# Kernel tuning notes

Hardware: AMD Instinct MI355X
Metric: run time of the kernel (lower is better)

Reference implementation:

```python
import jax, jax.numpy as jnp
import numpy as np

NP, NR, NK = 64, 8, 500          # problems, rollouts, candidate nodes
H, HEADS, VD = 256, 8, 8         # hidden_dim, heads, vars_dim
HD = H // HEADS                  # head_dim
CLIP = 10.0                      # tanh logit clipping
NEG_INF = -jnp.inf


def setup_inputs() -> dict:
    key = jax.random.key(0)
    ks = jax.random.split(key, 17)
    f = lambda k, s: jax.random.normal(k, s, dtype=jnp.float32)
    B = NP * NR
    s = 1.0 / np.sqrt(H)
    return {
        "X": f(ks[0], (NP, NK, H)),
        "K": f(ks[1], (HEADS, NP, NK, HD)),
        "V": f(ks[2], (HEADS, NP, NK, HD)),
        "query": f(ks[3], (B, H)),
        "state1": f(ks[4], (B, H)),
        "state2": f(ks[5], (B, H)),
        "varfeat": f(ks[6], (NP, VD, NK)),
        "mask": jax.random.uniform(ks[7], (NP, NR, NK)) < 0.1,
        "nn_Q": f(ks[8], (HEADS, H, HD)) * (1.0 / np.sqrt(HD)),
        "nn_O": f(ks[9], (H, H)) * s,
        "nn_A": f(ks[10], (VD, H)) * s,
        "nn_B": f(ks[11], (H,)) * s,
        "nn_W": f(ks[12], (H,)) * s,
        "W_ih": f(ks[13], (4 * H, H)) * s,
        "W_hh": f(ks[14], (4 * H, H)) * s,
        "b_ih": f(ks[15], (4 * H,)) * s,
        "b_hh": f(ks[16], (4 * H,)) * s,
    }


def _decode(X, K, V, query, state1, state2, varfeat, mask,
            nn_Q, nn_O, nn_A, nn_B, nn_W, W_ih, W_hh, b_ih, b_hh):
    B = query.shape[0]
    # --- LSTMCell (PyTorch gate order: i, f, g, o) ---
    gates = query @ W_ih.T + b_ih + state1 @ W_hh.T + b_hh
    i, fg, g, o = jnp.split(gates, 4, axis=1)
    c = jax.nn.sigmoid(fg) * state2 + jax.nn.sigmoid(i) * jnp.tanh(g)
    h = jax.nn.sigmoid(o) * jnp.tanh(c)
    # --- MultiHeadAttention (glimpse) ---
    q = h.reshape(NP, NR, H)
    Q = jnp.einsum('pqh,ahd->apqd', q, nn_Q)                    # [heads,NP,NR,HD]
    S = jnp.einsum('apqd,apkd->apqk', Q, K) * (1.0 / np.sqrt(HD))
    S = jnp.where(mask[None], NEG_INF, S)
    S = jax.nn.softmax(S, axis=-1)
    x = jnp.einsum('apqk,apkd->apqd', S, V)
    x = x.transpose(1, 2, 0, 3).reshape(NP, NR, H)              # [NP,NR,H]
    qm = x @ nn_O                                               # glimpse query
    # --- additive attention with variable features ---
    vf = jnp.einsum('pvk,vh->pkh', varfeat, nn_A) + nn_B        # [NP,NK,H]
    t = jnp.tanh(X[:, None] + vf[:, None] + qm[:, :, None])     # [NP,NR,NK,H]
    logit = jnp.einsum('pqkh,h->pqk', t, nn_W)
    logit = jnp.where(mask, NEG_INF, logit).reshape(B, NK)
    # --- choose (mode=1: greedy argmax) ---
    infeasible = logit == NEG_INF
    l = jnp.where(infeasible, NEG_INF, jnp.tanh(logit) * CLIP)
    chosen = jnp.argmax(l, axis=1)
    logp = jax.nn.log_softmax(l, axis=1)
    chosen_p = jnp.take_along_axis(logp, chosen[:, None], axis=1).squeeze(1)
    return h, c, chosen_p


def reference(X, K, V, query, state1, state2, varfeat, mask,
              nn_Q, nn_O, nn_A, nn_B, nn_W, W_ih, W_hh, b_ih, b_hh):
    return _decode(X, K, V, query, state1, state2, varfeat, mask,
                   nn_Q, nn_O, nn_A, nn_B, nn_W, W_ih, W_hh, b_ih, b_hh)
```

## Files before the change

kernel.cpp:

```cpp
#include <hip/hip_runtime.h>

#define NPP   64
#define NRR   8
#define NKK   500
#define HDIM  256
#define NHEAD 8
#define VDIM  8
#define HD    32
#define BTOT  512

__device__ __forceinline__ float fast_tanh(float x) {
  const float e = __expf(2.f * x);
  return 1.f - 2.f * __builtin_amdgcn_rcpf(e + 1.f);
}
__device__ __forceinline__ float fast_sig(float x) {
  return __builtin_amdgcn_rcpf(1.f + __expf(-x));
}

__global__ __launch_bounds__(128) void k_lstm5(
    const float* __restrict__ query, const float* __restrict__ state1,
    const float* __restrict__ state2,
    const float* __restrict__ W_ih, const float* __restrict__ W_hh,
    const float* __restrict__ b_ih, const float* __restrict__ b_hh,
    const unsigned char* __restrict__ maskb, int* __restrict__ flagp,
    float* __restrict__ out_h, float* __restrict__ out_c)
{
  __shared__ float Wt[32][36];
  __shared__ float At[32][68];
  __shared__ float gt[32][68];

  const int t  = threadIdx.x;
  const int hb = blockIdx.x;
  const int bb = blockIdx.y;

  if (flagp != nullptr && hb == 0 && bb == 0) {
    __shared__ int f;
    if (t == 0) f = 0;
    __syncthreads();
    int any = 0;
    for (int j = t; j < 2048; j += 128) any |= maskb[2 * j + 1];
    if (any) atomicOr(&f, 1);
    __syncthreads();
    if (t == 0) *flagp = f;
  }

  const int tr = t >> 4;
  const int tc = t & 15;

  const int grow = t >> 2;
  const int kseg = t & 3;
  const int wgrow = (grow >> 3) * HDIM + hb * 8 + (grow & 7);
  const int agrow0 = bb * 64 + grow;
  const int agrow1 = agrow0 + 32;

  float4 wr0, wr1, ar0, ar1, ar2, ar3;

#define LSTM_ISSUE(K0)                                                        \
  {                                                                           \
    const int k0_ = (K0);                                                     \
    const float* wsrc = (k0_ < 256)                                           \
        ? (W_ih + (size_t)wgrow * HDIM + k0_)                                 \
        : (W_hh + (size_t)wgrow * HDIM + (k0_ - 256));                        \
    wr0 = *reinterpret_cast<const float4*>(wsrc + kseg * 8);                  \
    wr1 = *reinterpret_cast<const float4*>(wsrc + kseg * 8 + 4);              \
    const float* asrc0 = (k0_ < 256)                                          \
        ? (query  + (size_t)agrow0 * HDIM + k0_)                              \
        : (state1 + (size_t)agrow0 * HDIM + (k0_ - 256));                     \
    ar0 = *reinterpret_cast<const float4*>(asrc0 + kseg * 8);                 \
    ar1 = *reinterpret_cast<const float4*>(asrc0 + kseg * 8 + 4);             \
    const float* asrc1 = (k0_ < 256)                                          \
        ? (query  + (size_t)agrow1 * HDIM + k0_)                              \
        : (state1 + (size_t)agrow1 * HDIM + (k0_ - 256));                     \
    ar2 = *reinterpret_cast<const float4*>(asrc1 + kseg * 8);                 \
    ar3 = *reinterpret_cast<const float4*>(asrc1 + kseg * 8 + 4);             \
  }

#define LSTM_WRITE()                                                          \
  {                                                                           \
    const float w0[4] = {wr0.x, wr0.y, wr0.z, wr0.w};                         \
    const float w1[4] = {wr1.x, wr1.y, wr1.z, wr1.w};                         \
    const float a0[4] = {ar0.x, ar0.y, ar0.z, ar0.w};                         \
    const float a1[4] = {ar1.x, ar1.y, ar1.z, ar1.w};                         \
    const float a2[4] = {ar2.x, ar2.y, ar2.z, ar2.w};                         \
    const float a3[4] = {ar3.x, ar3.y, ar3.z, ar3.w};                         \
    _Pragma("unroll")                                                         \
    for (int i = 0; i < 4; ++i) {                                             \
      Wt[kseg * 8 + i][grow]     = w0[i];                                     \
      Wt[kseg * 8 + 4 + i][grow] = w1[i];                                     \
      At[kseg * 8 + i][grow]     = a0[i];                                     \
      At[kseg * 8 + 4 + i][grow] = a1[i];                                     \
      At[kseg * 8 + i][grow + 32]     = a2[i];                                \
      At[kseg * 8 + 4 + i][grow + 32] = a3[i];                                \
    }                                                                         \
  }

  float acc[4][4];
#pragma unroll
  for (int i = 0; i < 4; ++i)
#pragma unroll
    for (int j = 0; j < 4; ++j) acc[i][j] = 0.f;

  LSTM_ISSUE(0);
  LSTM_WRITE();
  __syncthreads();

  for (int k0 = 0; k0 < 512; k0 += 32) {
    const bool more = (k0 + 32) < 512;
    if (more) LSTM_ISSUE(k0 + 32);

#pragma unroll 8
    for (int kk = 0; kk < 32; ++kk) {
      const float4 wv = *reinterpret_cast<const float4*>(&Wt[kk][tr * 4]);
      const float4 av = *reinterpret_cast<const float4*>(&At[kk][tc * 4]);
      const float w[4] = {wv.x, wv.y, wv.z, wv.w};
      const float a[4] = {av.x, av.y, av.z, av.w};
#pragma unroll
      for (int i = 0; i < 4; ++i)
#pragma unroll
        for (int j = 0; j < 4; ++j) acc[i][j] += w[i] * a[j];
    }
    __syncthreads();
    if (more) {
      LSTM_WRITE();
      __syncthreads();
    }
  }

#pragma unroll
  for (int i = 0; i < 4; ++i) {
    float4 v;
    v.x = acc[i][0]; v.y = acc[i][1]; v.z = acc[i][2]; v.w = acc[i][3];
    *reinterpret_cast<float4*>(&gt[tr * 4 + i][tc * 4]) = v;
  }
  __syncthreads();

#pragma unroll
  for (int it = 0; it < 4; ++it) {
    const int cell = t + 128 * it;
    const int h = cell & 7, b = cell >> 3;
    const int gh = hb * 8 + h;
    const int gb = bb * 64 + b;
    const float bi = b_ih[0 * HDIM + gh] + b_hh[0 * HDIM + gh];
    const float bf = b_ih[1 * HDIM + gh] + b_hh[1 * HDIM + gh];
    const float bg = b_ih[2 * HDIM + gh] + b_hh[2 * HDIM + gh];
    const float bo = b_ih[3 * HDIM + gh] + b_hh[3 * HDIM + gh];
    const float iv = fast_sig (gt[ 0 + h][b] + bi);
    const float fv = fast_sig (gt[ 8 + h][b] + bf);
    const float gv = fast_tanh(gt[16 + h][b] + bg);
    const float ov = fast_sig (gt[24 + h][b] + bo);
    const size_t off = (size_t)gb * HDIM + gh;
    const float c = fv * state2[off] + iv * gv;
    out_c[off] = c;
    out_h[off] = ov * fast_tanh(c);
  }
}

__global__ __launch_bounds__(512) void k_attn10(
    const float* __restrict__ Kt, const float* __restrict__ Vt,
    const float* __restrict__ nn_Q, const float* __restrict__ nn_O,
    const void* __restrict__ maskp, const int* __restrict__ flagp,
    const float* __restrict__ out_h, float* __restrict__ qm_slabs)
{
  const int p = blockIdx.x >> 3;
  const int a = blockIdx.x & 7;
  const int t = threadIdx.x;
  const int wave = t >> 6, lane = t & 63;

  __shared__ float hs[NRR][HDIM];
  __shared__ float Qs[NRR][36];
  __shared__ float Sb[NRR][512];
  __shared__ float pb[8][NRR][HD];
  __shared__ float xs[NRR][36];

  const float4 hv = reinterpret_cast<const float4*>(
      out_h + (size_t)p * NRR * HDIM)[t];

  const int flag = *flagp;

  const int kc = (t < NKK) ? t : (NKK - 1);
  const float4* kp4 = reinterpret_cast<const float4*>(
      Kt + (((size_t)a * NPP + p) * NKK + kc) * HD);
  float4 kreg[8];
#pragma unroll
  for (int j = 0; j < 8; ++j) kreg[j] = kp4[j];

  float maskv[NRR];
  {
    const unsigned char* mb = (const unsigned char*)maskp;
    const int* mi = (const int*)maskp;
#pragma unroll
    for (int r = 0; r < NRR; ++r) {
      const size_t mo = (size_t)(p * NRR + r) * NKK + kc;
      const bool mk = flag ? (mb[mo] != 0) : (mi[mo] != 0);
      maskv[r] = mk ? -INFINITY : 0.f;
    }
  }

  reinterpret_cast<float4*>(&hs[0][0])[t] = hv;
  __syncthreads();

  {
    const int r = wave;
    const int d4 = lane >> 3, ks = lane & 7;
    float qx = 0.f, qy = 0.f, qz = 0.f, qw = 0.f;
#pragma unroll
    for (int i = 0; i < 8; ++i) {
      const int hb = 32 * i + ks * 4;
      const float4 hv4 = *reinterpret_cast<const float4*>(&hs[r][hb]);
      const float hh[4] = {hv4.x, hv4.y, hv4.z, hv4.w};
      const float* nqb = nn_Q + ((size_t)a * HDIM + hb) * HD + d4 * 4;
#pragma unroll
      for (int jj = 0; jj < 4; ++jj) {
        const float4 wv = *reinterpret_cast<const float4*>(nqb + (size_t)jj * HD);
        qx += hh[jj] * wv.x; qy += hh[jj] * wv.y;
        qz += hh[jj] * wv.z; qw += hh[jj] * wv.w;
      }
    }
#pragma unroll
    for (int off = 1; off < 8; off <<= 1) {
      qx += __shfl_xor(qx, off, 64);
      qy += __shfl_xor(qy, off, 64);
      qz += __shfl_xor(qz, off, 64);
      qw += __shfl_xor(qw, off, 64);
    }
    if (ks == 0) {
      const float sc = 0.17677669529663687f;
      Qs[r][d4 * 4 + 0] = qx * sc; Qs[r][d4 * 4 + 1] = qy * sc;
      Qs[r][d4 * 4 + 2] = qz * sc; Qs[r][d4 * 4 + 3] = qw * sc;
    }
  }
  __syncthreads();

#pragma unroll
  for (int r = 0; r < NRR; ++r) {
    float s = 0.f;
#pragma unroll
    for (int j = 0; j < 8; ++j) {
      const float4 q = *reinterpret_cast<const float4*>(&Qs[r][j * 4]);
      const float4 k4 = kreg[j];
      s += q.x * k4.x + q.y * k4.y + q.z * k4.z + q.w * k4.w;
    }
    Sb[r][t] = (t < NKK) ? (s + maskv[r]) : -INFINITY;
  }

  const int kg = t >> 3;
  const int d4p = t & 7;
  float4 v4[8];
  {
    const float* vbase = Vt + ((size_t)a * NPP + p) * NKK * HD + d4p * 4;
#pragma unroll
    for (int j = 0; j < 8; ++j) {
      const int k = kg + 64 * j;
      v4[j] = (k < NKK)
          ? *reinterpret_cast<const float4*>(vbase + (size_t)k * HD)
          : make_float4(0.f, 0.f, 0.f, 0.f);
    }
  }
  __syncthreads();

  {
    const int r = wave;
    float lv[8], m = -INFINITY;
#pragma unroll
    for (int i = 0; i < 8; ++i) {
      lv[i] = Sb[r][lane + 64 * i];
      m = fmaxf(m, lv[i]);
    }
#pragma unroll
    for (int off = 32; off > 0; off >>= 1) m = fmaxf(m, __shfl_xor(m, off, 64));
    float ssum = 0.f;
#pragma unroll
    for (int i = 0; i < 8; ++i) {
      lv[i] = __expf(lv[i] - m);
      ssum += lv[i];
    }
#pragma unroll
    for (int off = 32; off > 0; off >>= 1) ssum += __shfl_xor(ssum, off, 64);
    const float inv = 1.f / ssum;
#pragma unroll
    for (int i = 0; i < 8; ++i) Sb[r][lane + 64 * i] = lv[i] * inv;
  }
  __syncthreads();

  {
    float4 acc4[NRR];
#pragma unroll
    for (int r = 0; r < NRR; ++r) acc4[r] = make_float4(0.f, 0.f, 0.f, 0.f);
#pragma unroll
    for (int j = 0; j < 8; ++j) {
      const float4 v = v4[j];
#pragma unroll
      for (int r = 0; r < NRR; ++r) {
        const float s = Sb[r][kg + 64 * j];
        acc4[r].x += s * v.x; acc4[r].y += s * v.y;
        acc4[r].z += s * v.z; acc4[r].w += s * v.w;
      }
    }
#pragma unroll
    for (int off = 8; off < 64; off <<= 1) {
#pragma unroll
      for (int r = 0; r < NRR; ++r) {
        acc4[r].x += __shfl_xor(acc4[r].x, off, 64);
        acc4[r].y += __shfl_xor(acc4[r].y, off, 64);
        acc4[r].z += __shfl_xor(acc4[r].z, off, 64);
        acc4[r].w += __shfl_xor(acc4[r].w, off, 64);
      }
    }
    if (lane < 8) {
#pragma unroll
      for (int r = 0; r < NRR; ++r)
        *reinterpret_cast<float4*>(&pb[wave][r][lane * 4]) = acc4[r];
    }
  }
  __syncthreads();

  if (t < 256) {
    const int r = t >> 5, d = t & 31;
    float s = 0.f;
#pragma unroll
    for (int w = 0; w < 8; ++w) s += pb[w][r][d];
    xs[r][d] = s;
  }
  __syncthreads();

  {
    const int j = t & 255, rr = t >> 8;
    float a0 = 0.f, a1 = 0.f, a2 = 0.f, a3 = 0.f;
#pragma unroll
    for (int d4 = 0; d4 < 8; ++d4) {
      const float4 x0 = *reinterpret_cast<const float4*>(&xs[rr * 4 + 0][d4 * 4]);
      const float4 x1 = *reinterpret_cast<const float4*>(&xs[rr * 4 + 1][d4 * 4]);
      const float4 x2 = *reinterpret_cast<const float4*>(&xs[rr * 4 + 2][d4 * 4]);
      const float4 x3 = *reinterpret_cast<const float4*>(&xs[rr * 4 + 3][d4 * 4]);
      const float c0[4] = {x0.x, x0.y, x0.z, x0.w};
      const float c1[4] = {x1.x, x1.y, x1.z, x1.w};
      const float c2[4] = {x2.x, x2.y, x2.z, x2.w};
      const float c3[4] = {x3.x, x3.y, x3.z, x3.w};
#pragma unroll
      for (int dd = 0; dd < 4; ++dd) {
        const float w = nn_O[((size_t)(a * HD + d4 * 4 + dd)) * HDIM + j];
        a0 += c0[dd] * w; a1 += c1[dd] * w;
        a2 += c2[dd] * w; a3 += c3[dd] * w;
      }
    }
    float* slab = qm_slabs + (size_t)a * BTOT * HDIM;
    slab[(size_t)(p * NRR + rr * 4 + 0) * HDIM + j] = a0;
    slab[(size_t)(p * NRR + rr * 4 + 1) * HDIM + j] = a1;
    slab[(size_t)(p * NRR + rr * 4 + 2) * HDIM + j] = a2;
    slab[(size_t)(p * NRR + rr * 4 + 3) * HDIM + j] = a3;
  }
}

__global__ __launch_bounds__(256) void k_qsum(
    const float* __restrict__ qm_slabs, const float* __restrict__ nn_B,
    float* __restrict__ qbg)
{
  const int idx = blockIdx.x * 256 + threadIdx.x;
  const int row = idx >> 6, h4 = idx & 63;
  float4 acc = *reinterpret_cast<const float4*>(nn_B + h4 * 4);
#pragma unroll
  for (int a = 0; a < NHEAD; ++a) {
    const float4 q = *reinterpret_cast<const float4*>(
        qm_slabs + (size_t)a * BTOT * HDIM + (size_t)row * HDIM + h4 * 4);
    acc.x += q.x; acc.y += q.y; acc.z += q.z; acc.w += q.w;
  }
  *reinterpret_cast<float4*>(qbg + (size_t)row * HDIM + h4 * 4) = acc;
}

__global__ __launch_bounds__(256) void k_logits7(
    const float* __restrict__ X, const float* __restrict__ varfeat,
    const float* __restrict__ nn_A, const float* __restrict__ nn_W,
    const float* __restrict__ qbg,
    const int* __restrict__ flagp, const void* __restrict__ maskp,
    float* __restrict__ pmax, float* __restrict__ psum)
{
  const int p  = blockIdx.x >> 5;
  const int kt = blockIdx.x & 31;
  const int t = threadIdx.x;
  const int wave = t >> 6, lane = t & 63;
  const int h0 = lane * 4;

  __shared__ float red[4][NRR][2];

  const unsigned char* mb = (const unsigned char*)maskp;
  const int* mi = (const int*)maskp;
  const int flag = *flagp;
  const bool mbyte = (flag != 0);

  const float4 w4 = *reinterpret_cast<const float4*>(nn_W + h0);
  float4 a4r[VDIM];
#pragma unroll
  for (int v = 0; v < VDIM; ++v)
    a4r[v] = *reinterpret_cast<const float4*>(nn_A + (size_t)v * HDIM + h0);
  float4 q4r[NRR];
#pragma unroll
  for (int r = 0; r < NRR; ++r)
    q4r[r] = *reinterpret_cast<const float4*>(
        qbg + (size_t)(p * NRR + r) * HDIM + h0);

  float rmax = -INFINITY, rsum = 0.f;

  for (int kk = 0; kk < 4; ++kk) {
    const int k = kt * 16 + wave * 4 + kk;
    if (k >= NKK) break;

    const float4 x4 = *reinterpret_cast<const float4*>(
        X + ((size_t)p * NKK + k) * HDIM + h0);
    float base0 = x4.x, base1 = x4.y, base2 = x4.z, base3 = x4.w;
#pragma unroll
    for (int v = 0; v < VDIM; ++v) {
      const float vv = varfeat[((size_t)p * VDIM + v) * NKK + k];
      base0 += vv * a4r[v].x; base1 += vv * a4r[v].y;
      base2 += vv * a4r[v].z; base3 += vv * a4r[v].w;
    }

    float acc[NRR];
#pragma unroll
    for (int r = 0; r < NRR; ++r) {
      acc[r] = fast_tanh(base0 + q4r[r].x) * w4.x
             + fast_tanh(base1 + q4r[r].y) * w4.y
             + fast_tanh(base2 + q4r[r].z) * w4.z
             + fast_tanh(base3 + q4r[r].w) * w4.w;
    }

    float v4[4];
    {
      float sw[8];
#pragma unroll
      for (int j = 0; j < 8; ++j) sw[j] = __shfl_xor(acc[j], 32, 64);
      const bool hi = (lane & 32) != 0;
#pragma unroll
      for (int j = 0; j < 4; ++j)
        v4[j] = hi ? (acc[j + 4] + sw[j + 4]) : (acc[j] + sw[j]);
    }
    float v2[2];
    {
      float sw[4];
#pragma unroll
      for (int j = 0; j < 4; ++j) sw[j] = __shfl_xor(v4[j], 16, 64);
      const bool hi = (lane & 16) != 0;
      v2[0] = hi ? (v4[2] + sw[2]) : (v4[0] + sw[0]);
      v2[1] = hi ? (v4[3] + sw[3]) : (v4[1] + sw[1]);
    }
    float w;
    {
      const float s0 = __shfl_xor(v2[0], 8, 64);
      const float s1 = __shfl_xor(v2[1], 8, 64);
      w = ((lane & 8) != 0) ? (v2[1] + s1) : (v2[0] + s0);
    }
    w += __shfl_xor(w, 4, 64);
    w += __shfl_xor(w, 2, 64);
    w += __shfl_xor(w, 1, 64);

    if ((lane & 7) == 0) {
      const int r = lane >> 3;
      const size_t mrow = (size_t)(p * NRR + r) * NKK + k;
      const bool mk = mbyte ? (mb[mrow] != 0) : (mi[mrow] != 0);
      const float l = mk ? -INFINITY : fast_tanh(w) * 10.0f;
      rmax = fmaxf(rmax, l);
      rsum += __expf(l - 10.f);
    }
  }

  if ((lane & 7) == 0) {
    red[wave][lane >> 3][0] = rmax;
    red[wave][lane >> 3][1] = rsum;
  }
  __syncthreads();
  if (t < NRR) {
    float m = red[0][t][0], s = red[0][t][1];
#pragma unroll
    for (int w = 1; w < 4; ++w) {
      m = fmaxf(m, red[w][t][0]);
      s += red[w][t][1];
    }
    pmax[(size_t)(p * NRR + t) * 32 + kt] = m;
    psum[(size_t)(p * NRR + t) * 32 + kt] = s;
  }
}

__global__ __launch_bounds__(64) void k_choose2(
    const float* __restrict__ pmax, const float* __restrict__ psum,
    float* __restrict__ out_p)
{
  const int b = blockIdx.x;
  const int lane = threadIdx.x;
  float m = (lane < 32) ? pmax[(size_t)b * 32 + lane] : -INFINITY;
  float s = (lane < 32) ? psum[(size_t)b * 32 + lane] : 0.f;
#pragma unroll
  for (int off = 16; off > 0; off >>= 1) {
    m = fmaxf(m, __shfl_xor(m, off, 64));
    s += __shfl_xor(s, off, 64);
  }
  if (lane == 0) out_p[b] = m - 10.f - logf(s);
}

__global__ __launch_bounds__(256) void k_fused(
    const float* __restrict__ X, const float* __restrict__ Kt,
    const float* __restrict__ Vt, const float* __restrict__ varfeat,
    const void* __restrict__ maskp,
    const float* __restrict__ nn_Q, const float* __restrict__ nn_O,
    const float* __restrict__ nn_A, const float* __restrict__ nn_B,
    const float* __restrict__ nn_W,
    const float* __restrict__ out_h, float* __restrict__ out_p)
{
  const int p = blockIdx.x >> 3;
  const int r = blockIdx.x & 7;
  const int t = threadIdx.x;
  const int wave = t >> 6, lane = t & 63;

  __shared__ float hs[HDIM];
  __shared__ float Qs[NHEAD][HD];
  __shared__ float Sb[NHEAD][NKK];
  __shared__ float xs[HDIM];
  __shared__ float qs[HDIM];
  __shared__ float As2[HDIM][VDIM];
  __shared__ float Ws[HDIM];
  __shared__ float lsb[NKK];
  __shared__ int   mask_any;

  const unsigned char* mb = (const unsigned char*)maskp;
  if (t == 0) mask_any = 0;
  __syncthreads();
  {
    int any = 0;
    for (int j = t; j < 2048; j += 256) any |= mb[2 * j + 1];
    if (any) atomicOr(&mask_any, 1);
  }
  for (int idx = t; idx < VDIM * HDIM; idx += 256)
    As2[idx & 255][idx >> 8] = nn_A[idx];
  Ws[t] = nn_W[t];
  hs[t] = out_h[(size_t)(p * NRR + r) * HDIM + t];
  __syncthreads();
  const bool mbyte = (mask_any != 0);
  const int* mi = (const int*)maskp;
  const size_t mrow = (size_t)(p * NRR + r) * NKK;
  {
    const int a = t >> 5, d = t & 31;
    const float* nq = nn_Q + (size_t)a * HDIM * HD + d;
    float acc = 0.f;
    for (int h = 0; h < HDIM; ++h) acc += hs[h] * nq[(size_t)h * HD];
    Qs[a][d] = acc * 0.17677669529663687f;
  }
  __syncthreads();
  for (int k = t; k < NKK; k += 256) {
    const bool mk = mbyte ? (mb[mrow + k] != 0) : (mi[mrow + k] != 0);
#pragma unroll
    for (int a = 0; a < NHEAD; ++a) {
      const float4* kr4 = reinterpret_cast<const float4*>(
          Kt + (((size_t)a * NPP + p) * NKK + k) * HD);
      float s = 0.f;
#pragma unroll
      for (int d4 = 0; d4 < HD / 4; ++d4) {
        const float4 u = kr4[d4];
        s += Qs[a][4 * d4] * u.x + Qs[a][4 * d4 + 1] * u.y
           + Qs[a][4 * d4 + 2] * u.z + Qs[a][4 * d4 + 3] * u.w;
      }
      Sb[a][k] = mk ? -INFINITY : s;
    }
  }
  __syncthreads();
  for (int aa = 0; aa < 2; ++aa) {
    const int a = wave * 2 + aa;
    float m = -INFINITY;
    for (int k = lane; k < NKK; k += 64) m = fmaxf(m, Sb[a][k]);
#pragma unroll
    for (int off = 32; off > 0; off >>= 1) m = fmaxf(m, __shfl_xor(m, off, 64));
    float ssum = 0.f;
    for (int k = lane; k < NKK; k += 64) {
      const float e = expf(Sb[a][k] - m);
      Sb[a][k] = e; ssum += e;
    }
#pragma unroll
    for (int off = 32; off > 0; off >>= 1) ssum += __shfl_xor(ssum, off, 64);
    const float inv = 1.f / ssum;
    for (int k = lane; k < NKK; k += 64) Sb[a][k] *= inv;
  }
  __syncthreads();
  {
    const int a = t >> 5, d = t & 31;
    const float* vb = Vt + ((size_t)a * NPP + p) * NKK * HD + d;
    float acc = 0.f;
    for (int k = 0; k < NKK; ++k) acc += Sb[a][k] * vb[(size_t)k * HD];
    xs[a * HD + d] = acc;
  }
  __syncthreads();
  {
    float acc = 0.f;
    for (int i = 0; i < HDIM; ++i) acc += xs[i] * nn_O[(size_t)i * HDIM + t];
    qs[t] = acc + nn_B[t];
  }
  __syncthreads();
  for (int k = t; k < NKK; k += 256) {
    float vfv[VDIM];
#pragma unroll
    for (int v = 0; v < VDIM; ++v)
      vfv[v] = varfeat[((size_t)p * VDIM + v) * NKK + k];
    const float4* xp4 = reinterpret_cast<const float4*>(
        X + ((size_t)p * NKK + k) * HDIM);
    float acc = 0.f;
    for (int h4 = 0; h4 < HDIM / 4; ++h4) {
      const float4 ux = xp4[h4];
      const float xv[4] = {ux.x, ux.y, ux.z, ux.w};
#pragma unroll
      for (int j = 0; j < 4; ++j) {
        const int h = 4 * h4 + j;
        float base = xv[j] + qs[h];
        const float4 a0 = *reinterpret_cast<const float4*>(&As2[h][0]);
        const float4 a1 = *reinterpret_cast<const float4*>(&As2[h][4]);
        base += vfv[0] * a0.x + vfv[1] * a0.y + vfv[2] * a0.z + vfv[3] * a0.w
              + vfv[4] * a1.x + vfv[5] * a1.y + vfv[6] * a1.z + vfv[7] * a1.w;
        acc += tanhf(base) * Ws[h];
      }
    }
    lsb[k] = acc;
  }
  __syncthreads();
  for (int k = t; k < NKK; k += 256) {
    const bool mk = mbyte ? (mb[mrow + k] != 0) : (mi[mrow + k] != 0);
    lsb[k] = mk ? -INFINITY : tanhf(lsb[k]) * 10.0f;
  }
  __syncthreads();
  if (wave == 0) {
    float m = -INFINITY;
    for (int k = lane; k < NKK; k += 64) m = fmaxf(m, lsb[k]);
#pragma unroll
    for (int off = 32; off > 0; off >>= 1) m = fmaxf(m, __shfl_xor(m, off, 64));
    float s = 0.f;
    for (int k = lane; k < NKK; k += 64) s += expf(lsb[k] - m);
#pragma unroll
    for (int off = 32; off > 0; off >>= 1) s += __shfl_xor(s, off, 64);
    if (lane == 0) out_p[p * NRR + r] = -logf(s);
  }
}

extern "C" void kernel_launch(void* const* d_in, const int* in_sizes, int n_in,
                              void* d_out, int out_size, void* d_ws, size_t ws_size,
                              hipStream_t stream)
{
  const float* X       = (const float*)d_in[0];
  const float* Kt      = (const float*)d_in[1];
  const float* Vt      = (const float*)d_in[2];
  const float* query   = (const float*)d_in[3];
  const float* state1  = (const float*)d_in[4];
  const float* state2  = (const float*)d_in[5];
  const float* varfeat = (const float*)d_in[6];
  const void*  maskp   = d_in[7];
  const float* nn_Q    = (const float*)d_in[8];
  const float* nn_O    = (const float*)d_in[9];
  const float* nn_A    = (const float*)d_in[10];
  const float* nn_B    = (const float*)d_in[11];
  const float* nn_W    = (const float*)d_in[12];
  const float* W_ih    = (const float*)d_in[13];
  const float* W_hh    = (const float*)d_in[14];
  const float* b_ih    = (const float*)d_in[15];
  const float* b_hh    = (const float*)d_in[16];

  float* out   = (float*)d_out;
  float* out_h = out;
  float* out_c = out + (size_t)BTOT * HDIM;
  float* out_p = out + (size_t)2 * BTOT * HDIM;

  const size_t flag_bytes = 256;
  const size_t qm8_bytes  = (size_t)NHEAD * BTOT * HDIM * 4;
  const size_t qbg_bytes  = (size_t)BTOT * HDIM * 4;
  const size_t part_bytes = (size_t)BTOT * 32 * 4;
  const size_t need = flag_bytes + qm8_bytes + qbg_bytes + 2 * part_bytes;

  if (ws_size >= need) {
    int*   flagp = (int*)d_ws;
    float* qmw  = (float*)((char*)d_ws + flag_bytes);
    float* qbg  = (float*)((char*)d_ws + flag_bytes + qm8_bytes);
    float* pmax = (float*)((char*)d_ws + flag_bytes + qm8_bytes + qbg_bytes);
    float* psum = (float*)((char*)d_ws + flag_bytes + qm8_bytes + qbg_bytes
                           + part_bytes);

    hipLaunchKernelGGL(k_lstm5, dim3(32, 8), dim3(128), 0, stream,
                       query, state1, state2, W_ih, W_hh, b_ih, b_hh,
                       (const unsigned char*)maskp, flagp, out_h, out_c);
    hipLaunchKernelGGL(k_attn10, dim3(NPP * NHEAD), dim3(512), 0, stream,
                       Kt, Vt, nn_Q, nn_O, maskp, flagp, out_h, qmw);
    hipLaunchKernelGGL(k_qsum, dim3(128), dim3(256), 0, stream,
                       qmw, nn_B, qbg);
    hipLaunchKernelGGL(k_logits7, dim3(NPP * 32), dim3(256), 0, stream,
                       X, varfeat, nn_A, nn_W, qbg, flagp, maskp,
                       pmax, psum);
    hipLaunchKernelGGL(k_choose2, dim3(BTOT), dim3(64), 0, stream,
                       pmax, psum, out_p);
  } else {
    hipLaunchKernelGGL(k_lstm5, dim3(32, 8), dim3(128), 0, stream,
                       query, state1, state2, W_ih, W_hh, b_ih, b_hh,
                       (const unsigned char*)maskp, nullptr, out_h, out_c);
    hipLaunchKernelGGL(k_fused, dim3(NPP * NRR), dim3(256), 0, stream,
                       X, Kt, Vt, varfeat, maskp,
                       nn_Q, nn_O, nn_A, nn_B, nn_W,
                       out_h, out_p);
  }
}
```

Measured before the change: 227.1 us.

## Fold qsum and choose kernels into last-block epilogues and retile LSTM GEMM

Removes the separate k_qsum and k_choose2 launches. The last attention block per problem (found with an atomic counter) now sums the head slabs plus the bias, and the last logits block per problem does the log-softmax finish. The LSTM kernel is retiled to 256 threads with a 32x32 tile and 2x2 per-thread outputs, dropping its register prefetch double-buffering. The attention kernel hoists V and nn_O loads earlier and pins them in registers. Counters are reset in the LSTM kernel. This cuts launch overhead at the cost of atomics, fences and a smaller LSTM tile with less reuse.

```diff
diff --git a/kernel.cpp b/kernel.cpp
--- a/kernel.cpp
+++ b/kernel.cpp
@@ -17,17 +17,21 @@
   return __builtin_amdgcn_rcpf(1.f + __expf(-x));
 }
 
-__global__ __launch_bounds__(128) void k_lstm5(
+#define PIN1(x)  asm volatile("" :: "v"(x))
+#define PIN4(v)  asm volatile("" :: "v"((v).x), "v"((v).y), "v"((v).z), "v"((v).w))
+
+__global__ __launch_bounds__(256) void k_lstm3(
     const float* __restrict__ query, const float* __restrict__ state1,
     const float* __restrict__ state2,
     const float* __restrict__ W_ih, const float* __restrict__ W_hh,
     const float* __restrict__ b_ih, const float* __restrict__ b_hh,
     const unsigned char* __restrict__ maskb, int* __restrict__ flagp,
+    int* __restrict__ cnts,
     float* __restrict__ out_h, float* __restrict__ out_c)
 {
-  __shared__ float Wt[32][36];
-  __shared__ float At[32][68];
-  __shared__ float gt[32][68];
+  __shared__ float Wt[32][33];
+  __shared__ float At[32][33];
+  __shared__ float gt[32][33];
 
   const int t  = threadIdx.x;
   const int hb = blockIdx.x;
@@ -36,110 +40,59 @@
   if (flagp != nullptr && hb == 0 && bb == 0) {
     __shared__ int f;
     if (t == 0) f = 0;
+    if (cnts != nullptr && t < 128) cnts[t] = 0;
     __syncthreads();
     int any = 0;
-    for (int j = t; j < 2048; j += 128) any |= maskb[2 * j + 1];
+    for (int j = t; j < 2048; j += 256) any |= maskb[2 * j + 1];
     if (any) atomicOr(&f, 1);
     __syncthreads();
     if (t == 0) *flagp = f;
   }
 
-  const int tr = t >> 4;
-  const int tc = t & 15;
-
-  const int grow = t >> 2;
-  const int kseg = t & 3;
-  const int wgrow = (grow >> 3) * HDIM + hb * 8 + (grow & 7);
-  const int agrow0 = bb * 64 + grow;
-  const int agrow1 = agrow0 + 32;
-
-  float4 wr0, wr1, ar0, ar1, ar2, ar3;
-
-#define LSTM_ISSUE(K0)                                                        \
-  {                                                                           \
-    const int k0_ = (K0);                                                     \
-    const float* wsrc = (k0_ < 256)                                           \
-        ? (W_ih + (size_t)wgrow * HDIM + k0_)                                 \
-        : (W_hh + (size_t)wgrow * HDIM + (k0_ - 256));                        \
-    wr0 = *reinterpret_cast<const float4*>(wsrc + kseg * 8);                  \
-    wr1 = *reinterpret_cast<const float4*>(wsrc + kseg * 8 + 4);              \
-    const float* asrc0 = (k0_ < 256)                                          \
-        ? (query  + (size_t)agrow0 * HDIM + k0_)                              \
-        : (state1 + (size_t)agrow0 * HDIM + (k0_ - 256));                     \
-    ar0 = *reinterpret_cast<const float4*>(asrc0 + kseg * 8);                 \
-    ar1 = *reinterpret_cast<const float4*>(asrc0 + kseg * 8 + 4);             \
-    const float* asrc1 = (k0_ < 256)                                          \
-        ? (query  + (size_t)agrow1 * HDIM + k0_)                              \
-        : (state1 + (size_t)agrow1 * HDIM + (k0_ - 256));                     \
-    ar2 = *reinterpret_cast<const float4*>(asrc1 + kseg * 8);                 \
-    ar3 = *reinterpret_cast<const float4*>(asrc1 + kseg * 8 + 4);             \
-  }
-
-#define LSTM_WRITE()                                                          \
-  {                                                                           \
-    const float w0[4] = {wr0.x, wr0.y, wr0.z, wr0.w};                         \
-    const float w1[4] = {wr1.x, wr1.y, wr1.z, wr1.w};                         \
-    const float a0[4] = {ar0.x, ar0.y, ar0.z, ar0.w};                         \
-    const float a1[4] = {ar1.x, ar1.y, ar1.z, ar1.w};                         \
-    const float a2[4] = {ar2.x, ar2.y, ar2.z, ar2.w};                         \
-    const float a3[4] = {ar3.x, ar3.y, ar3.z, ar3.w};                         \
-    _Pragma("unroll")                                                         \
-    for (int i = 0; i < 4; ++i) {                                             \
-      Wt[kseg * 8 + i][grow]     = w0[i];                                     \
-      Wt[kseg * 8 + 4 + i][grow] = w1[i];                                     \
-      At[kseg * 8 + i][grow]     = a0[i];                                     \
-      At[kseg * 8 + 4 + i][grow] = a1[i];                                     \
-      At[kseg * 8 + i][grow + 32]     = a2[i];                                \
-      At[kseg * 8 + 4 + i][grow + 32] = a3[i];                                \
-    }                                                                         \
-  }
-
-  float acc[4][4];
-#pragma unroll
-  for (int i = 0; i < 4; ++i)
-#pragma unroll
-    for (int j = 0; j < 4; ++j) acc[i][j] = 0.f;
-
-  LSTM_ISSUE(0);
-  LSTM_WRITE();
-  __syncthreads();
+  const int trow = t >> 4;
+  const int tcol = t & 15;
+
+  float acc00 = 0.f, acc01 = 0.f, acc10 = 0.f, acc11 = 0.f;
+
+  const int wrow = t >> 3, wk4 = t & 7;
+  const int wpart = wrow >> 3, whh = wrow & 7;
+  const int wgrow = wpart * HDIM + hb * 8 + whh;
+  const int agrow = bb * 32 + wrow;
 
   for (int k0 = 0; k0 < 512; k0 += 32) {
-    const bool more = (k0 + 32) < 512;
-    if (more) LSTM_ISSUE(k0 + 32);
+    __syncthreads();
+    {
+      const float* wsrc = (k0 < 256) ? (W_ih + (size_t)wgrow * HDIM + k0)
+                                     : (W_hh + (size_t)wgrow * HDIM + (k0 - 256));
+      const float4 wv = *reinterpret_cast<const float4*>(wsrc + wk4 * 4);
+      Wt[wk4 * 4 + 0][wrow] = wv.x; Wt[wk4 * 4 + 1][wrow] = wv.y;
+      Wt[wk4 * 4 + 2][wrow] = wv.z; Wt[wk4 * 4 + 3][wrow] = wv.w;
+
+      const float* asrc = (k0 < 256) ? (query  + (size_t)agrow * HDIM + k0)
+                                     : (state1 + (size_t)agrow * HDIM + (k0 - 256));
+      const float4 av = *reinterpret_cast<const float4*>(asrc + wk4 * 4);
+      At[wk4 * 4 + 0][wrow] = av.x; At[wk4 * 4 + 1][wrow] = av.y;
+      At[wk4 * 4 + 2][wrow] = av.z; At[wk4 * 4 + 3][wrow] = av.w;
+    }
+    __syncthreads();
 
 #pragma unroll 8
     for (int kk = 0; kk < 32; ++kk) {
-      const float4 wv = *reinterpret_cast<const float4*>(&Wt[kk][tr * 4]);
-      const float4 av = *reinterpret_cast<const float4*>(&At[kk][tc * 4]);
-      const float w[4] = {wv.x, wv.y, wv.z, wv.w};
-      const float a[4] = {av.x, av.y, av.z, av.w};
-#pragma unroll
-      for (int i = 0; i < 4; ++i)
-#pragma unroll
-        for (int j = 0; j < 4; ++j) acc[i][j] += w[i] * a[j];
-    }
-    __syncthreads();
-    if (more) {
-      LSTM_WRITE();
-      __syncthreads();
-    }
-  }
-
-#pragma unroll
-  for (int i = 0; i < 4; ++i) {
-    float4 v;
-    v.x = acc[i][0]; v.y = acc[i][1]; v.z = acc[i][2]; v.w = acc[i][3];
-    *reinterpret_cast<float4*>(&gt[tr * 4 + i][tc * 4]) = v;
-  }
-  __syncthreads();
-
-#pragma unroll
-  for (int it = 0; it < 4; ++it) {
-    const int cell = t + 128 * it;
-    const int h = cell & 7, b = cell >> 3;
+      const float w0 = Wt[kk][trow], w1 = Wt[kk][trow + 16];
+      const float a0 = At[kk][tcol], a1 = At[kk][tcol + 16];
+      acc00 += w0 * a0; acc01 += w0 * a1;
+      acc10 += w1 * a0; acc11 += w1 * a1;
+    }
+  }
+
+  gt[trow][tcol] = acc00;      gt[trow][tcol + 16] = acc01;
+  gt[trow + 16][tcol] = acc10; gt[trow + 16][tcol + 16] = acc11;
+  __syncthreads();
+
+  {
+    const int h = t & 7, b = t >> 3;
     const int gh = hb * 8 + h;
-    const int gb = bb * 64 + b;
+    const int gb = bb * 32 + b;
     const float bi = b_ih[0 * HDIM + gh] + b_hh[0 * HDIM + gh];
     const float bf = b_ih[1 * HDIM + gh] + b_hh[1 * HDIM + gh];
     const float bg = b_ih[2 * HDIM + gh] + b_hh[2 * HDIM + gh];
@@ -155,11 +108,14 @@
   }
 }
 
-__global__ __launch_bounds__(512) void k_attn10(
+__global__ __launch_bounds__(512, 4) void k_attn11(
     const float* __restrict__ Kt, const float* __restrict__ Vt,
     const float* __restrict__ nn_Q, const float* __restrict__ nn_O,
+    const float* __restrict__ nn_B,
     const void* __restrict__ maskp, const int* __restrict__ flagp,
-    const float* __restrict__ out_h, float* __restrict__ qm_slabs)
+    int* __restrict__ cnta,
+    const float* __restrict__ out_h, float* __restrict__ qm_slabs,
+    float* __restrict__ qbg)
 {
   const int p = blockIdx.x >> 3;
   const int a = blockIdx.x & 7;
@@ -171,6 +127,7 @@
   __shared__ float Sb[NRR][512];
   __shared__ float pb[8][NRR][HD];
   __shared__ float xs[NRR][36];
+  __shared__ int   lastf;
 
   const float4 hv = reinterpret_cast<const float4*>(
       out_h + (size_t)p * NRR * HDIM)[t];
@@ -184,6 +141,20 @@
 #pragma unroll
   for (int j = 0; j < 8; ++j) kreg[j] = kp4[j];
 
+  const int kg = t >> 3;
+  const int d4p = t & 7;
+  float4 v4[8];
+  {
+    const float* vbase = Vt + ((size_t)a * NPP + p) * NKK * HD + d4p * 4;
+#pragma unroll
+    for (int j = 0; j < 8; ++j) {
+      const int k = kg + 64 * j;
+      v4[j] = (k < NKK)
+          ? *reinterpret_cast<const float4*>(vbase + (size_t)k * HD)
+          : make_float4(0.f, 0.f, 0.f, 0.f);
+    }
+  }
+
   float maskv[NRR];
   {
     const unsigned char* mb = (const unsigned char*)maskp;
@@ -197,6 +168,11 @@
   }
 
   reinterpret_cast<float4*>(&hs[0][0])[t] = hv;
+
+#pragma unroll
+  for (int j = 0; j < 8; ++j) { PIN4(kreg[j]); PIN4(v4[j]); }
+#pragma unroll
+  for (int r = 0; r < NRR; ++r) PIN1(maskv[r]);
   __syncthreads();
 
   {
@@ -243,18 +219,12 @@
     Sb[r][t] = (t < NKK) ? (s + maskv[r]) : -INFINITY;
   }
 
-  const int kg = t >> 3;
-  const int d4p = t & 7;
-  float4 v4[8];
-  {
-    const float* vbase = Vt + ((size_t)a * NPP + p) * NKK * HD + d4p * 4;
-#pragma unroll
-    for (int j = 0; j < 8; ++j) {
-      const int k = kg + 64 * j;
-      v4[j] = (k < NKK)
-          ? *reinterpret_cast<const float4*>(vbase + (size_t)k * HD)
-          : make_float4(0.f, 0.f, 0.f, 0.f);
-    }
+  const int j8 = t & 255;
+  float orr[32];
+  {
+    const float* ob = nn_O + (size_t)(a * HD) * HDIM + j8;
+#pragma unroll
+    for (int d = 0; d < 32; ++d) orr[d] = ob[(size_t)d * HDIM];
   }
   __syncthreads();
 
@@ -324,7 +294,7 @@
   __syncthreads();
 
   {
-    const int j = t & 255, rr = t >> 8;
+    const int rr = t >> 8;
     float a0 = 0.f, a1 = 0.f, a2 = 0.f, a3 = 0.f;
 #pragma unroll
     for (int d4 = 0; d4 < 8; ++d4) {
@@ -338,41 +308,48 @@
       const float c3[4] = {x3.x, x3.y, x3.z, x3.w};
 #pragma unroll
       for (int dd = 0; dd < 4; ++dd) {
-        const float w = nn_O[((size_t)(a * HD + d4 * 4 + dd)) * HDIM + j];
+        const float w = orr[d4 * 4 + dd];
         a0 += c0[dd] * w; a1 += c1[dd] * w;
         a2 += c2[dd] * w; a3 += c3[dd] * w;
       }
     }
     float* slab = qm_slabs + (size_t)a * BTOT * HDIM;
-    slab[(size_t)(p * NRR + rr * 4 + 0) * HDIM + j] = a0;
-    slab[(size_t)(p * NRR + rr * 4 + 1) * HDIM + j] = a1;
-    slab[(size_t)(p * NRR + rr * 4 + 2) * HDIM + j] = a2;
-    slab[(size_t)(p * NRR + rr * 4 + 3) * HDIM + j] = a3;
+    slab[(size_t)(p * NRR + rr * 4 + 0) * HDIM + j8] = a0;
+    slab[(size_t)(p * NRR + rr * 4 + 1) * HDIM + j8] = a1;
+    slab[(size_t)(p * NRR + rr * 4 + 2) * HDIM + j8] = a2;
+    slab[(size_t)(p * NRR + rr * 4 + 3) * HDIM + j8] = a3;
+  }
+
+  __syncthreads();
+  if (t == 0) {
+    __threadfence();
+    lastf = (atomicAdd(&cnta[p], 1) == NHEAD - 1) ? 1 : 0;
+  }
+  __syncthreads();
+  if (lastf) {
+    __threadfence();
+    const int row = t >> 6, h4 = t & 63;
+    float4 acc = *reinterpret_cast<const float4*>(nn_B + h4 * 4);
+#pragma unroll
+    for (int a2 = 0; a2 < NHEAD; ++a2) {
+      const float4 q = *reinterpret_cast<const float4*>(
+          qm_slabs + (size_t)a2 * BTOT * HDIM +
+          (size_t)(p * NRR + row) * HDIM + h4 * 4);
+      acc.x += q.x; acc.y += q.y; acc.z += q.z; acc.w += q.w;
+    }
+    *reinterpret_cast<float4*>(
+        qbg + (size_t)(p * NRR + row) * HDIM + h4 * 4) = acc;
   }
 }
 
-__global__ __launch_bounds__(256) void k_qsum(
-    const float* __restrict__ qm_slabs, const float* __restrict__ nn_B,
-    float* __restrict__ qbg)
-{
-  const int idx = blockIdx.x * 256 + threadIdx.x;
-  const int row = idx >> 6, h4 = idx & 63;
-  float4 acc = *reinterpret_cast<const float4*>(nn_B + h4 * 4);
-#pragma unroll
-  for (int a = 0; a < NHEAD; ++a) {
-    const float4 q = *reinterpret_cast<const float4*>(
-        qm_slabs + (size_t)a * BTOT * HDIM + (size_t)row * HDIM + h4 * 4);
-    acc.x += q.x; acc.y += q.y; acc.z += q.z; acc.w += q.w;
-  }
-  *reinterpret_cast<float4*>(qbg + (size_t)row * HDIM + h4 * 4) = acc;
-}
-
-__global__ __launch_bounds__(256) void k_logits7(
+__global__ __launch_bounds__(256) void k_logits8(
     const float* __restrict__ X, const float* __restrict__ varfeat,
     const float* __restrict__ nn_A, const float* __restrict__ nn_W,
     const float* __restrict__ qbg,
     const int* __restrict__ flagp, const void* __restrict__ maskp,
-    float* __restrict__ pmax, float* __restrict__ psum)
+    int* __restrict__ cntl,
+    float* __restrict__ pmax, float* __restrict__ psum,
+    float* __restrict__ out_p)
 {
   const int p  = blockIdx.x >> 5;
   const int kt = blockIdx.x & 31;
@@ -381,6 +358,7 @@
   const int h0 = lane * 4;
 
   __shared__ float red[4][NRR][2];
+  __shared__ int   lastl;
 
   const unsigned char* mb = (const unsigned char*)maskp;
   const int* mi = (const int*)maskp;
@@ -423,7 +401,7 @@
              + fast_tanh(base3 + q4r[r].w) * w4.w;
     }
 
-    float v4[4];
+    float v4r[4];
     {
       float sw[8];
 #pragma unroll
@@ -431,16 +409,16 @@
       const bool hi = (lane & 32) != 0;
 #pragma unroll
       for (int j = 0; j < 4; ++j)
-        v4[j] = hi ? (acc[j + 4] + sw[j + 4]) : (acc[j] + sw[j]);
+        v4r[j] = hi ? (acc[j + 4] + sw[j + 4]) : (acc[j] + sw[j]);
     }
     float v2[2];
     {
       float sw[4];
 #pragma unroll
-      for (int j = 0; j < 4; ++j) sw[j] = __shfl_xor(v4[j], 16, 64);
+      for (int j = 0; j < 4; ++j) sw[j] = __shfl_xor(v4r[j], 16, 64);
       const bool hi = (lane & 16) != 0;
-      v2[0] = hi ? (v4[2] + sw[2]) : (v4[0] + sw[0]);
-      v2[1] = hi ? (v4[3] + sw[3]) : (v4[1] + sw[1]);
+      v2[0] = hi ? (v4r[2] + sw[2]) : (v4r[0] + sw[0]);
+      v2[1] = hi ? (v4r[3] + sw[3]) : (v4r[1] + sw[1]);
     }
     float w;
     {
@@ -477,22 +455,27 @@
     pmax[(size_t)(p * NRR + t) * 32 + kt] = m;
     psum[(size_t)(p * NRR + t) * 32 + kt] = s;
   }
-}
-
-__global__ __launch_bounds__(64) void k_choose2(
-    const float* __restrict__ pmax, const float* __restrict__ psum,
-    float* __restrict__ out_p)
-{
-  const int b = blockIdx.x;
-  const int lane = threadIdx.x;
-  float m = (lane < 32) ? pmax[(size_t)b * 32 + lane] : -INFINITY;
-  float s = (lane < 32) ? psum[(size_t)b * 32 + lane] : 0.f;
-#pragma unroll
-  for (int off = 16; off > 0; off >>= 1) {
-    m = fmaxf(m, __shfl_xor(m, off, 64));
-    s += __shfl_xor(s, off, 64);
-  }
-  if (lane == 0) out_p[b] = m - 10.f - logf(s);
+
+  __syncthreads();
+  if (t == 0) {
+    __threadfence();
+    lastl = (atomicAdd(&cntl[p], 1) == 31) ? 1 : 0;
+  }
+  __syncthreads();
+  if (lastl) {
+    __threadfence();
+    if (t < 256) {
+      const int r = t >> 5, k2 = t & 31;
+      float m = pmax[(size_t)(p * NRR + r) * 32 + k2];
+      float s = psum[(size_t)(p * NRR + r) * 32 + k2];
+#pragma unroll
+      for (int off = 16; off > 0; off >>= 1) {
+        m = fmaxf(m, __shfl_xor(m, off, 64));
+        s += __shfl_xor(s, off, 64);
+      }
+      if (k2 == 0) out_p[p * NRR + r] = m - 10.f - logf(s);
+    }
+  }
 }
 
 __global__ __launch_bounds__(256) void k_fused(
@@ -661,36 +644,38 @@
   float* out_c = out + (size_t)BTOT * HDIM;
   float* out_p = out + (size_t)2 * BTOT * HDIM;
 
-  const size_t flag_bytes = 256;
+  const size_t hdr_bytes  = 1024;
   const size_t qm8_bytes  = (size_t)NHEAD * BTOT * HDIM * 4;
   const size_t qbg_bytes  = (size_t)BTOT * HDIM * 4;
   const size_t part_bytes = (size_t)BTOT * 32 * 4;
-  const size_t need = flag_bytes + qm8_bytes + qbg_bytes + 2 * part_bytes;
+  const size_t need = hdr_bytes + qm8_bytes + qbg_bytes + 2 * part_bytes;
 
   if (ws_size >= need) {
     int*   flagp = (int*)d_ws;
-    float* qmw  = (float*)((char*)d_ws + flag_bytes);
-    float* qbg  = (float*)((char*)d_ws + flag_bytes + qm8_bytes);
-    float* pmax = (float*)((char*)d_ws + flag_bytes + qm8_bytes + qbg_bytes);
-    float* psum = (float*)((char*)d_ws + flag_bytes + qm8_bytes + qbg_bytes
+    int*   cnts  = (int*)((char*)d_ws + 256);
+    int*   cnta  = cnts;
+    int*   cntl  = (int*)((char*)d_ws + 512);
+    float* qmw  = (float*)((char*)d_ws + hdr_bytes);
+    float* qbg  = (float*)((char*)d_ws + hdr_bytes + qm8_bytes);
+    float* pmax = (float*)((char*)d_ws + hdr_bytes + qm8_bytes + qbg_bytes);
+    float* psum = (float*)((char*)d_ws + hdr_bytes + qm8_bytes + qbg_bytes
                            + part_bytes);
 
-    hipLaunchKernelGGL(k_lstm5, dim3(32, 8), dim3(128), 0, stream,
+    hipLaunchKernelGGL(k_lstm3, dim3(32, 16), dim3(256), 0, stream,
                        query, state1, state2, W_ih, W_hh, b_ih, b_hh,
-                       (const unsigned char*)maskp, flagp, out_h, out_c);
-    hipLaunchKernelGGL(k_attn10, dim3(NPP * NHEAD), dim3(512), 0, stream,
-                       Kt, Vt, nn_Q, nn_O, maskp, flagp, out_h, qmw);
-    hipLaunchKernelGGL(k_qsum, dim3(128), dim3(256), 0, stream,
-                       qmw, nn_B, qbg);
-    hipLaunchKernelGGL(k_logits7, dim3(NPP * 32), dim3(256), 0, stream,
-                       X, varfeat, nn_A, nn_W, qbg, flagp, maskp,
-                       pmax, psum);
-    hipLaunchKernelGGL(k_choose2, dim3(BTOT), dim3(64), 0, stream,
+                       (const unsigned char*)maskp, flagp, cnts,
+                       out_h, out_c);
+    hipLaunchKernelGGL(k_attn11, dim3(NPP * NHEAD), dim3(512), 0, stream,
+                       Kt, Vt, nn_Q, nn_O, nn_B, maskp, flagp, cnta,
+                       out_h, qmw, qbg);
+    hipLaunchKernelGGL(k_logits8, dim3(NPP * 32), dim3(256), 0, stream,
+                       X, varfeat, nn_A, nn_W, qbg, flagp, maskp, cntl,
                        pmax, psum, out_p);
   } else {
-    hipLaunchKernelGGL(k_lstm5, dim3(32, 8), dim3(128), 0, stream,
+    hipLaunchKernelGGL(k_lstm3, dim3(32, 16), dim3(256), 0, stream,
                        query, state1, state2, W_ih, W_hh, b_ih, b_hh,
-                       (const unsigned char*)maskp, nullptr, out_h, out_c);
+                       (const unsigned char*)maskp, nullptr, nullptr,
+                       out_h, out_c);
     hipLaunchKernelGGL(k_fused, dim3(NPP * NRR), dim3(256), 0, stream,
                        X, Kt, Vt, varfeat, maskp,
                        nn_Q, nn_O, nn_A, nn_B, nn_W,
```

Result: slower. 369.0 us (+62.5%).
